# Optimization experiments

Measured on AMD Instinct MI355X. Metric: run time of the kernel, lower is better.

Reference implementation:

```python
import jax, jax.numpy as jnp
import numpy as np

B, S, D, H = 2, 2048, 1024, 16
DK = D // H


def setup_inputs() -> dict:
    key = jax.random.key(0)
    ks = jax.random.split(key, 11)
    scale = 1.0 / np.sqrt(D)
    inp = {
        "q": jax.random.normal(ks[0], (B, S, D), jnp.float32),
        "k": jax.random.normal(ks[1], (B, S, D), jnp.float32),
        "v": jax.random.normal(ks[2], (B, S, D), jnp.float32),
        "mask": jnp.tril(jnp.ones((S, S), jnp.int32))[None, None],  # causal [1,1,S,S]
        "wq": jax.random.normal(ks[3], (D, D), jnp.float32) * scale,
        "bq": jnp.zeros((D,), jnp.float32),
        "wk": jax.random.normal(ks[4], (D, D), jnp.float32) * scale,
        "bk": jnp.zeros((D,), jnp.float32),
        "wv": jax.random.normal(ks[5], (D, D), jnp.float32) * scale,
        "bv": jnp.zeros((D,), jnp.float32),
        "wo": jax.random.normal(ks[6], (D, D), jnp.float32) * scale,
        "bo": jnp.zeros((D,), jnp.float32),
    }
    return inp


def _split_heads(x):  # [B,S,D] -> [B,H,S,DK]
    return x.reshape(B, S, H, DK).transpose(0, 2, 1, 3)


def reference(q, k, v, mask, wq, bq, wk, bk, wv, bv, wo, bo):
    # projections (nn.Linear: x @ W.T + b)
    query = _split_heads(q @ wq.T + bq)
    key_ = _split_heads(k @ wk.T + bk)
    value = _split_heads(v @ wv.T + bv)
    # scaled dot-product attention, full [B,H,S,S] scores as in source
    scores = jnp.einsum('bhqd,bhkd->bhqk', query, key_) / np.sqrt(DK)
    scores = jnp.where(mask == 0, jnp.float32(-1e9), scores)
    attn = jax.nn.softmax(scores, axis=-1)
    out = jnp.einsum('bhqk,bhkd->bhqd', attn, value)
    out = out.transpose(0, 2, 1, 3).reshape(B, S, D)
    x = out @ wo.T + bo
    return x, attn
```

## Files before the change

### kernel.cpp

```cpp
#include <hip/hip_runtime.h>
#include <hip/hip_bf16.h>

typedef __attribute__((ext_vector_type(8))) __bf16 bf16x8;
typedef __attribute__((ext_vector_type(4))) __bf16 bf16x4;
typedef __attribute__((ext_vector_type(4))) float f32x4;

#define MFMA16(a, b, c) __builtin_amdgcn_mfma_f32_16x16x32_bf16((a), (b), (c), 0, 0, 0)

#define SEQ 2048
#define DIM 1024

__device__ __forceinline__ void gload_lds16(const __bf16* g, __bf16* l) {
  __builtin_amdgcn_global_load_lds(
      (const __attribute__((address_space(1))) void*)g,
      (__attribute__((address_space(3))) void*)l, 16, 0, 0);
}

__global__ __launch_bounds__(256) void cvt_bf16(
    const float* __restrict__ q, const float* __restrict__ k, const float* __restrict__ v,
    const float* __restrict__ wq, const float* __restrict__ wk, const float* __restrict__ wv,
    const float* __restrict__ wo,
    __bf16* __restrict__ qb, __bf16* __restrict__ kb, __bf16* __restrict__ vb,
    __bf16* __restrict__ wqb, __bf16* __restrict__ wkb, __bf16* __restrict__ wvb,
    __bf16* __restrict__ wob) {
  int a = blockIdx.y;
  const float* src = (a == 0) ? q : (a == 1) ? k : (a == 2) ? v
                    : (a == 3) ? wq : (a == 4) ? wk : (a == 5) ? wv : wo;
  __bf16* dst = (a == 0) ? qb : (a == 1) ? kb : (a == 2) ? vb
               : (a == 3) ? wqb : (a == 4) ? wkb : (a == 5) ? wvb : wob;
  size_t n = (a < 3) ? (size_t)(2 * SEQ * DIM) : (size_t)(DIM * DIM);
  size_t i = ((size_t)blockIdx.x * 256 + threadIdx.x) * 8;
  if (i >= n) return;
  float4 f0 = *(const float4*)&src[i];
  float4 f1 = *(const float4*)&src[i + 4];
  bf16x8 o = {(__bf16)f0.x, (__bf16)f0.y, (__bf16)f0.z, (__bf16)f0.w,
              (__bf16)f1.x, (__bf16)f1.y, (__bf16)f1.z, (__bf16)f1.w};
  *(bf16x8*)&dst[i] = o;
}

__global__ __launch_bounds__(256) void qkv_gemm(
    const __bf16* __restrict__ qI, const __bf16* __restrict__ kI, const __bf16* __restrict__ vI,
    const __bf16* __restrict__ wqI, const __bf16* __restrict__ wkI, const __bf16* __restrict__ wvI,
    const float* __restrict__ bqI, const float* __restrict__ bkI, const float* __restrict__ bvI,
    __bf16* __restrict__ Qp, __bf16* __restrict__ Kp, __bf16* __restrict__ Vt) {
  const int N = 1024, K = 1024;
  int z = blockIdx.z;
  const __bf16* A = (z == 0) ? qI : (z == 1) ? kI : vI;
  const __bf16* W = (z == 0) ? wqI : (z == 1) ? wkI : wvI;
  const float* bias = (z == 0) ? bqI : (z == 1) ? bkI : bvI;

  __shared__ __bf16 As[2][128 * 32];
  __shared__ __bf16 Bs[2][128 * 32];

  int tid = threadIdx.x;
  int wave = tid >> 6, lane = tid & 63;
  int quad = lane >> 4, l16 = lane & 15;
  int wm = (wave >> 1) * 64, wn = (wave & 1) * 64;
  int m0 = blockIdx.y * 128, n0 = blockIdx.x * 128;

  int srow = wave * 16 + (lane >> 2);
  int scol = (lane & 3) * 8;
  const __bf16* Ab = &A[(size_t)(m0 + srow) * K + scol];
  const __bf16* Wb = &W[(size_t)(n0 + srow) * K + scol];
  int lo = wave * 512;

  f32x4 acc[4][4] = {};

  {
    gload_lds16(Ab, &As[0][lo]);
    gload_lds16(Ab + (size_t)64 * K, &As[0][lo + 2048]);
    gload_lds16(Wb, &Bs[0][lo]);
    gload_lds16(Wb + (size_t)64 * K, &Bs[0][lo + 2048]);
  }

  int buf = 0;
  for (int k0 = 0; k0 < K; k0 += 32) {
    __syncthreads();
    if (k0 + 32 < K) {
      int nb = buf ^ 1;
      gload_lds16(Ab + k0 + 32, &As[nb][lo]);
      gload_lds16(Ab + (size_t)64 * K + k0 + 32, &As[nb][lo + 2048]);
      gload_lds16(Wb + k0 + 32, &Bs[nb][lo]);
      gload_lds16(Wb + (size_t)64 * K + k0 + 32, &Bs[nb][lo + 2048]);
    }
    const __bf16* as = &As[buf][0];
    const __bf16* bs = &Bs[buf][0];
    bf16x8 af[4], bfv[4];
#pragma unroll
    for (int i = 0; i < 4; i++) af[i] = *(const bf16x8*)&as[(wm + i * 16 + l16) * 32 + quad * 8];
#pragma unroll
    for (int j = 0; j < 4; j++) bfv[j] = *(const bf16x8*)&bs[(wn + j * 16 + l16) * 32 + quad * 8];
#pragma unroll
    for (int i = 0; i < 4; i++)
#pragma unroll
      for (int j = 0; j < 4; j++) acc[i][j] = MFMA16(af[i], bfv[j], acc[i][j]);
    buf ^= 1;
  }

#pragma unroll
  for (int j = 0; j < 4; j++) {
    int col = n0 + wn + j * 16 + l16;
    float bj = bias[col];
    if (z == 2) {
#pragma unroll
      for (int i = 0; i < 4; i++) {
        int row0 = m0 + wm + i * 16 + quad * 4;
        int bb = row0 >> 11, s = row0 & 2047;
        bf16x4 pv = {(__bf16)(acc[i][j][0] + bj), (__bf16)(acc[i][j][1] + bj),
                     (__bf16)(acc[i][j][2] + bj), (__bf16)(acc[i][j][3] + bj)};
        *(bf16x4*)&Vt[((size_t)bb * 1024 + col) * SEQ + s] = pv;
      }
    } else {
      __bf16* C = (z == 0) ? Qp : Kp;
      float scale = (z == 0) ? 0.125f : 1.0f;
#pragma unroll
      for (int i = 0; i < 4; i++)
#pragma unroll
        for (int r = 0; r < 4; r++) {
          int row = m0 + wm + i * 16 + quad * 4 + r;
          C[(size_t)row * N + col] = (__bf16)((acc[i][j][r] + bj) * scale);
        }
    }
  }
}

__global__ __launch_bounds__(256) void out_gemm(
    const __bf16* __restrict__ A, const __bf16* __restrict__ W,
    const float* __restrict__ bias, float* __restrict__ C) {
  const int N = 1024, K = 1024;
  __shared__ __bf16 As[2][128 * 32];
  __shared__ __bf16 Bs[2][128 * 32];

  int tid = threadIdx.x;
  int wave = tid >> 6, lane = tid & 63;
  int quad = lane >> 4, l16 = lane & 15;
  int wm = (wave >> 1) * 64, wn = (wave & 1) * 64;
  int m0 = blockIdx.y * 128, n0 = blockIdx.x * 128;

  int srow = wave * 16 + (lane >> 2);
  int scol = (lane & 3) * 8;
  const __bf16* Ab = &A[(size_t)(m0 + srow) * K + scol];
  const __bf16* Wb = &W[(size_t)(n0 + srow) * K + scol];
  int lo = wave * 512;

  f32x4 acc[4][4] = {};

  {
    gload_lds16(Ab, &As[0][lo]);
    gload_lds16(Ab + (size_t)64 * K, &As[0][lo + 2048]);
    gload_lds16(Wb, &Bs[0][lo]);
    gload_lds16(Wb + (size_t)64 * K, &Bs[0][lo + 2048]);
  }

  int buf = 0;
  for (int k0 = 0; k0 < K; k0 += 32) {
    __syncthreads();
    if (k0 + 32 < K) {
      int nb = buf ^ 1;
      gload_lds16(Ab + k0 + 32, &As[nb][lo]);
      gload_lds16(Ab + (size_t)64 * K + k0 + 32, &As[nb][lo + 2048]);
      gload_lds16(Wb + k0 + 32, &Bs[nb][lo]);
      gload_lds16(Wb + (size_t)64 * K + k0 + 32, &Bs[nb][lo + 2048]);
    }
    const __bf16* as = &As[buf][0];
    const __bf16* bs = &Bs[buf][0];
    bf16x8 af[4], bfv[4];
#pragma unroll
    for (int i = 0; i < 4; i++) af[i] = *(const bf16x8*)&as[(wm + i * 16 + l16) * 32 + quad * 8];
#pragma unroll
    for (int j = 0; j < 4; j++) bfv[j] = *(const bf16x8*)&bs[(wn + j * 16 + l16) * 32 + quad * 8];
#pragma unroll
    for (int i = 0; i < 4; i++)
#pragma unroll
      for (int j = 0; j < 4; j++) acc[i][j] = MFMA16(af[i], bfv[j], acc[i][j]);
    buf ^= 1;
  }

#pragma unroll
  for (int j = 0; j < 4; j++) {
    int col = n0 + wn + j * 16 + l16;
    float bj = bias[col];
#pragma unroll
    for (int i = 0; i < 4; i++)
#pragma unroll
      for (int r = 0; r < 4; r++) {
        int row = m0 + wm + i * 16 + quad * 4 + r;
        C[(size_t)row * N + col] = acc[i][j][r] + bj;
      }
  }
}

__global__ __launch_bounds__(256) void attn_fused(
    const __bf16* __restrict__ Qp, const __bf16* __restrict__ Kp,
    const __bf16* __restrict__ Vt, float* __restrict__ attn,
    __bf16* __restrict__ Oc) {
  int bh = blockIdx.y;
  int b = bh >> 4;
  int hofs = (bh & 15) * 64;
  int q0 = blockIdx.x * 64;

  int tid = threadIdx.x;
  int wave = tid >> 6, lane = tid & 63;
  int quad = lane >> 4, l16 = lane & 15;

  __shared__ __bf16 Ks[128][72];
  __shared__ __bf16 Vts[64][136];
  __shared__ __bf16 Ps[64][136];

  const size_t rowbase = (size_t)b * SEQ;
  const size_t vtbase = (size_t)bh * 64 * SEQ;

  int qg = q0 + wave * 16 + l16;

  const __bf16* qpp = &Qp[(rowbase + qg) * DIM + hofs + quad * 8];
  bf16x8 qfrag0 = *(const bf16x8*)qpp;
  bf16x8 qfrag1 = *(const bf16x8*)(qpp + 32);

  float m_i = -1e30f, l_i = 0.f;
  int ktmax = (q0 + 63) >> 7;

  for (int kt = 0; kt <= ktmax; kt++) {
    int k0 = kt << 7;
    __syncthreads();
#pragma unroll
    for (int it = 0; it < 4; it++) {
      int flat = tid * 8 + it * 2048;
      int r = flat >> 6, c = flat & 63;
      *(bf16x8*)&Ks[r][c] = *(const bf16x8*)&Kp[(rowbase + k0 + r) * DIM + hofs + c];
    }
    __syncthreads();

    f32x4 sacc[8] = {};
#pragma unroll
    for (int t = 0; t < 8; t++) {
      bf16x8 a0 = *(bf16x8*)&Ks[t * 16 + l16][quad * 8];
      bf16x8 a1 = *(bf16x8*)&Ks[t * 16 + l16][32 + quad * 8];
      sacc[t] = MFMA16(a0, qfrag0, sacc[t]);
      sacc[t] = MFMA16(a1, qfrag1, sacc[t]);
    }

    bool diag = (kt == ktmax);
    float sv[32];
    float mx = -1e30f;
#pragma unroll
    for (int t = 0; t < 8; t++)
#pragma unroll
      for (int r = 0; r < 4; r++) {
        float s = sacc[t][r];
        int k = k0 + t * 16 + quad * 4 + r;
        if (diag && k > qg) s = -1e30f;
        sv[t * 4 + r] = s;
        mx = fmaxf(mx, s);
      }
    mx = fmaxf(mx, __shfl_xor(mx, 16));
    mx = fmaxf(mx, __shfl_xor(mx, 32));
    float mn = fmaxf(m_i, mx);
    float sum = 0.f;
#pragma unroll
    for (int i = 0; i < 32; i++) sum += __expf(sv[i] - mn);
    sum += __shfl_xor(sum, 16);
    sum += __shfl_xor(sum, 32);
    l_i = l_i * __expf(m_i - mn) + sum;
    m_i = mn;
  }

  float rl = 1.f / l_i;
  f32x4 oacc[4] = {};
  float* attn_bh = attn + (size_t)bh * SEQ * SEQ;
  float* attn_row = attn_bh + (size_t)qg * SEQ;

  for (int kt = 0; kt < SEQ / 128; kt++) {
    int k0 = kt << 7;
    if (kt <= ktmax) {
      __syncthreads();
#pragma unroll
      for (int it = 0; it < 4; it++) {
        int flat = tid * 8 + it * 2048;
        int r = flat >> 6, c = flat & 63;
        *(bf16x8*)&Ks[r][c] = *(const bf16x8*)&Kp[(rowbase + k0 + r) * DIM + hofs + c];
        int d = flat >> 7, c2 = flat & 127;
        *(bf16x8*)&Vts[d][c2] = *(const bf16x8*)&Vt[vtbase + (size_t)d * SEQ + k0 + c2];
      }
      __syncthreads();

      f32x4 sacc[8] = {};
#pragma unroll
      for (int t = 0; t < 8; t++) {
        bf16x8 a0 = *(bf16x8*)&Ks[t * 16 + l16][quad * 8];
        bf16x8 a1 = *(bf16x8*)&Ks[t * 16 + l16][32 + quad * 8];
        sacc[t] = MFMA16(a0, qfrag0, sacc[t]);
        sacc[t] = MFMA16(a1, qfrag1, sacc[t]);
      }

      bool diag = (kt == ktmax);
#pragma unroll
      for (int t = 0; t < 8; t++) {
        float p[4];
#pragma unroll
        for (int r = 0; r < 4; r++) {
          int k = k0 + t * 16 + quad * 4 + r;
          float s = sacc[t][r];
          p[r] = (!diag || k <= qg) ? __expf(s - m_i) * rl : 0.f;
        }
        *(float4*)&attn_row[k0 + t * 16 + quad * 4] = make_float4(p[0], p[1], p[2], p[3]);
        bf16x4 ph = {(__bf16)p[0], (__bf16)p[1], (__bf16)p[2], (__bf16)p[3]};
        *(bf16x4*)&Ps[wave * 16 + l16][t * 16 + quad * 4] = ph;
      }
      __syncthreads();

#pragma unroll
      for (int ks = 0; ks < 4; ks++) {
        bf16x8 a = *(bf16x8*)&Ps[wave * 16 + l16][ks * 32 + quad * 8];
#pragma unroll
        for (int dt = 0; dt < 4; dt++) {
          bf16x8 bb = *(bf16x8*)&Vts[dt * 16 + l16][ks * 32 + quad * 8];
          oacc[dt] = MFMA16(a, bb, oacc[dt]);
        }
      }
    } else {
      float4 z4 = make_float4(0.f, 0.f, 0.f, 0.f);
#pragma unroll
      for (int i = 0; i < 8; i++) {
        int f4 = tid + i * 256;
        int r = f4 >> 5;
        int c = (f4 & 31) * 4;
        *(float4*)&attn_bh[(size_t)(q0 + r) * SEQ + k0 + c] = z4;
      }
    }
  }

#pragma unroll
  for (int dt = 0; dt < 4; dt++)
#pragma unroll
    for (int rr = 0; rr < 4; rr++) {
      int row = q0 + wave * 16 + quad * 4 + rr;
      Oc[(rowbase + row) * DIM + hofs + dt * 16 + l16] = (__bf16)oacc[dt][rr];
    }
}

extern "C" void kernel_launch(void* const* d_in, const int* in_sizes, int n_in,
                              void* d_out, int out_size, void* d_ws, size_t ws_size,
                              hipStream_t stream) {
  const float* q = (const float*)d_in[0];
  const float* k = (const float*)d_in[1];
  const float* v = (const float*)d_in[2];
  const float* wq = (const float*)d_in[4];
  const float* bq = (const float*)d_in[5];
  const float* wk = (const float*)d_in[6];
  const float* bk = (const float*)d_in[7];
  const float* wv = (const float*)d_in[8];
  const float* bv = (const float*)d_in[9];
  const float* wo = (const float*)d_in[10];
  const float* bo = (const float*)d_in[11];

  float* xout = (float*)d_out;
  float* attn = xout + (size_t)2 * SEQ * DIM;

  const size_t NBS = (size_t)2 * SEQ * DIM;
  const size_t NW = (size_t)DIM * DIM;

  __bf16* Qp = (__bf16*)d_ws;
  __bf16* Kp = Qp + NBS;
  __bf16* Vt = Kp + NBS;
  __bf16* Oc = Vt + NBS;
  __bf16* qb = Oc + NBS;
  __bf16* kb = qb + NBS;
  __bf16* vb = kb + NBS;
  __bf16* wqb = vb + NBS;
  __bf16* wkb = wqb + NW;
  __bf16* wvb = wkb + NW;
  __bf16* wob = wvb + NW;

  dim3 blk(256);

  dim3 g0(2048, 7);
  cvt_bf16<<<g0, blk, 0, stream>>>(q, k, v, wq, wk, wv, wo,
                                   qb, kb, vb, wqb, wkb, wvb, wob);

  dim3 g1(8, 32, 3);
  qkv_gemm<<<g1, blk, 0, stream>>>(qb, kb, vb, wqb, wkb, wvb, bq, bk, bv, Qp, Kp, Vt);

  dim3 g2(32, 32);
  attn_fused<<<g2, blk, 0, stream>>>(Qp, Kp, Vt, attn, Oc);

  dim3 g3(8, 32);
  out_gemm<<<g3, blk, 0, stream>>>(Oc, wob, bo, xout);
}
```

Before: 762.9 us.

## Double-buffer K tiles via registers, load V fragments directly, reverse query-block order

```diff
diff --git a/kernel.cpp b/kernel.cpp
--- a/kernel.cpp
+++ b/kernel.cpp
@@ -197,14 +197,13 @@
   int bh = blockIdx.y;
   int b = bh >> 4;
   int hofs = (bh & 15) * 64;
-  int q0 = blockIdx.x * 64;
+  int q0 = (31 - blockIdx.x) * 64;
 
   int tid = threadIdx.x;
   int wave = tid >> 6, lane = tid & 63;
   int quad = lane >> 4, l16 = lane & 15;
 
-  __shared__ __bf16 Ks[128][72];
-  __shared__ __bf16 Vts[64][136];
+  __shared__ __bf16 Ks[2][128][72];
   __shared__ __bf16 Ps[64][136];
 
   const size_t rowbase = (size_t)b * SEQ;
@@ -216,25 +215,36 @@
   bf16x8 qfrag0 = *(const bf16x8*)qpp;
   bf16x8 qfrag1 = *(const bf16x8*)(qpp + 32);
 
+  const __bf16* vb = Vt + vtbase + (size_t)l16 * SEQ + quad * 8;
+
+  const int sr = tid >> 3, sc = (tid & 7) * 8;
+
   float m_i = -1e30f, l_i = 0.f;
   int ktmax = (q0 + 63) >> 7;
+
+  bf16x8 kreg[4];
+
+#pragma unroll
+  for (int it = 0; it < 4; it++)
+    kreg[it] = *(const bf16x8*)&Kp[(rowbase + sr + it * 32) * DIM + hofs + sc];
+#pragma unroll
+  for (int it = 0; it < 4; it++) *(bf16x8*)&Ks[0][sr + it * 32][sc] = kreg[it];
+  int cur = 0;
 
   for (int kt = 0; kt <= ktmax; kt++) {
     int k0 = kt << 7;
     __syncthreads();
-#pragma unroll
-    for (int it = 0; it < 4; it++) {
-      int flat = tid * 8 + it * 2048;
-      int r = flat >> 6, c = flat & 63;
-      *(bf16x8*)&Ks[r][c] = *(const bf16x8*)&Kp[(rowbase + k0 + r) * DIM + hofs + c];
-    }
-    __syncthreads();
+    if (kt < ktmax) {
+#pragma unroll
+      for (int it = 0; it < 4; it++)
+        kreg[it] = *(const bf16x8*)&Kp[(rowbase + k0 + 128 + sr + it * 32) * DIM + hofs + sc];
+    }
 
     f32x4 sacc[8] = {};
 #pragma unroll
     for (int t = 0; t < 8; t++) {
-      bf16x8 a0 = *(bf16x8*)&Ks[t * 16 + l16][quad * 8];
-      bf16x8 a1 = *(bf16x8*)&Ks[t * 16 + l16][32 + quad * 8];
+      bf16x8 a0 = *(bf16x8*)&Ks[cur][t * 16 + l16][quad * 8];
+      bf16x8 a1 = *(bf16x8*)&Ks[cur][t * 16 + l16][32 + quad * 8];
       sacc[t] = MFMA16(a0, qfrag0, sacc[t]);
       sacc[t] = MFMA16(a1, qfrag1, sacc[t]);
     }
@@ -262,6 +272,12 @@
     sum += __shfl_xor(sum, 32);
     l_i = l_i * __expf(m_i - mn) + sum;
     m_i = mn;
+
+    if (kt < ktmax) {
+#pragma unroll
+      for (int it = 0; it < 4; it++) *(bf16x8*)&Ks[cur ^ 1][sr + it * 32][sc] = kreg[it];
+      cur ^= 1;
+    }
   }
 
   float rl = 1.f / l_i;
@@ -269,25 +285,35 @@
   float* attn_bh = attn + (size_t)bh * SEQ * SEQ;
   float* attn_row = attn_bh + (size_t)qg * SEQ;
 
+#pragma unroll
+  for (int it = 0; it < 4; it++)
+    kreg[it] = *(const bf16x8*)&Kp[(rowbase + sr + it * 32) * DIM + hofs + sc];
+  __syncthreads();
+#pragma unroll
+  for (int it = 0; it < 4; it++) *(bf16x8*)&Ks[0][sr + it * 32][sc] = kreg[it];
+  cur = 0;
+
   for (int kt = 0; kt < SEQ / 128; kt++) {
     int k0 = kt << 7;
     if (kt <= ktmax) {
       __syncthreads();
-#pragma unroll
-      for (int it = 0; it < 4; it++) {
-        int flat = tid * 8 + it * 2048;
-        int r = flat >> 6, c = flat & 63;
-        *(bf16x8*)&Ks[r][c] = *(const bf16x8*)&Kp[(rowbase + k0 + r) * DIM + hofs + c];
-        int d = flat >> 7, c2 = flat & 127;
-        *(bf16x8*)&Vts[d][c2] = *(const bf16x8*)&Vt[vtbase + (size_t)d * SEQ + k0 + c2];
-      }
-      __syncthreads();
+      if (kt < ktmax) {
+#pragma unroll
+        for (int it = 0; it < 4; it++)
+          kreg[it] = *(const bf16x8*)&Kp[(rowbase + k0 + 128 + sr + it * 32) * DIM + hofs + sc];
+      }
+      bf16x8 vfr[4][4];
+#pragma unroll
+      for (int ks = 0; ks < 4; ks++)
+#pragma unroll
+        for (int dt = 0; dt < 4; dt++)
+          vfr[ks][dt] = *(const bf16x8*)(vb + (size_t)(dt * 16) * SEQ + k0 + ks * 32);
 
       f32x4 sacc[8] = {};
 #pragma unroll
       for (int t = 0; t < 8; t++) {
-        bf16x8 a0 = *(bf16x8*)&Ks[t * 16 + l16][quad * 8];
-        bf16x8 a1 = *(bf16x8*)&Ks[t * 16 + l16][32 + quad * 8];
+        bf16x8 a0 = *(bf16x8*)&Ks[cur][t * 16 + l16][quad * 8];
+        bf16x8 a1 = *(bf16x8*)&Ks[cur][t * 16 + l16][32 + quad * 8];
         sacc[t] = MFMA16(a0, qfrag0, sacc[t]);
         sacc[t] = MFMA16(a1, qfrag1, sacc[t]);
       }
@@ -306,16 +332,19 @@
         bf16x4 ph = {(__bf16)p[0], (__bf16)p[1], (__bf16)p[2], (__bf16)p[3]};
         *(bf16x4*)&Ps[wave * 16 + l16][t * 16 + quad * 4] = ph;
       }
-      __syncthreads();
+      asm volatile("s_waitcnt lgkmcnt(0)" ::: "memory");
 
 #pragma unroll
       for (int ks = 0; ks < 4; ks++) {
         bf16x8 a = *(bf16x8*)&Ps[wave * 16 + l16][ks * 32 + quad * 8];
 #pragma unroll
-        for (int dt = 0; dt < 4; dt++) {
-          bf16x8 bb = *(bf16x8*)&Vts[dt * 16 + l16][ks * 32 + quad * 8];
-          oacc[dt] = MFMA16(a, bb, oacc[dt]);
-        }
+        for (int dt = 0; dt < 4; dt++) oacc[dt] = MFMA16(a, vfr[ks][dt], oacc[dt]);
+      }
+
+      if (kt < ktmax) {
+#pragma unroll
+        for (int it = 0; it < 4; it++) *(bf16x8*)&Ks[cur ^ 1][sr + it * 32][sc] = kreg[it];
+        cur ^= 1;
       }
     } else {
       float4 z4 = make_float4(0.f, 0.f, 0.f, 0.f);
```

Result: slower. 816.9 us (+7.1%).
